# Kernel tuning notes

Hardware: AMD Instinct MI355X
Metric: run time of the kernel (lower is better)

Reference implementation:

```python
import jax, jax.numpy as jnp
import numpy as np

B, S, D, H = 2, 2048, 1024, 16
DK = D // H


def setup_inputs() -> dict:
    key = jax.random.key(0)
    ks = jax.random.split(key, 12)
    s = 0.02
    return {
        "q": jax.random.normal(ks[0], (B, S, D), jnp.float32),
        "k": jax.random.normal(ks[1], (B, S, D), jnp.float32),
        "v": jax.random.normal(ks[2], (B, S, D), jnp.float32),
        "mask": jax.random.randint(ks[3], (1, 1, S, S), 0, 2, jnp.int32),
        "Wq": jax.random.normal(ks[4], (D, D), jnp.float32) * s,
        "bq": jnp.zeros((D,), jnp.float32),
        "Wk": jax.random.normal(ks[5], (D, D), jnp.float32) * s,
        "bk": jnp.zeros((D,), jnp.float32),
        "Wv": jax.random.normal(ks[6], (D, D), jnp.float32) * s,
        "bv": jnp.zeros((D,), jnp.float32),
        "Wo": jax.random.normal(ks[7], (D, D), jnp.float32) * s,
        "bo": jnp.zeros((D,), jnp.float32),
    }


def reference(q, k, v, mask, Wq, bq, Wk, bk, Wv, bv, Wo, bo):
    # linear projections (torch Linear: x @ W.T + b)
    qp = q @ Wq.T + bq
    kp = k @ Wk.T + bk
    vp = v @ Wv.T + bv
    # [B, S, D] -> [B, H, S, DK]
    split = lambda x: x.reshape(B, S, H, DK).transpose(0, 2, 1, 3)
    qh, kh, vh = split(qp), split(kp), split(vp)
    scale = 1.0 / jnp.sqrt(jnp.float32(DK))
    attn = jnp.einsum('bhsd,bhtd->bhst', qh, kh) * scale  # [B,H,S,S]
    attn = jnp.where(mask == 0, jnp.float32(-1e9), attn)
    attn = jax.nn.softmax(attn, axis=-1)
    out = jnp.einsum('bhst,bhtd->bhsd', attn, vh)  # [B,H,S,DK]
    concat = out.transpose(0, 2, 1, 3).reshape(B, S, D)
    return concat @ Wo.T + bo
```

## Files before the change

### kernel.cpp

```cpp
#include <hip/hip_runtime.h>
#include <hip/hip_bf16.h>


using bf16x8 = __attribute__((ext_vector_type(8))) short;
using f32x4  = __attribute__((ext_vector_type(4))) float;

constexpr int Bc = 2, Sc = 2048, Dc = 1024, Hc = 16, DKc = 64;
constexpr int Mc = Bc * Sc;
#define LOG2E_OVER_SQRTDK 0.18033688011112042f

__device__ __forceinline__ void lds_load16(const void* g, void* l) {
  __builtin_amdgcn_global_load_lds(
      (const __attribute__((address_space(1))) unsigned int*)g,
      (__attribute__((address_space(3))) unsigned int*)l, 16, 0, 0);
}

__device__ __forceinline__ unsigned pack2bf(float a, float b) {
  union { __hip_bfloat16 h; unsigned short s; } ua, ub;
  ua.h = __float2bfloat16(a);
  ub.h = __float2bfloat16(b);
  return (unsigned)ua.s | ((unsigned)ub.s << 16);
}

__global__ void cast3_kernel(const float* __restrict__ a, const float* __restrict__ b,
                             const float* __restrict__ c, __hip_bfloat16* __restrict__ oa,
                             __hip_bfloat16* __restrict__ ob, __hip_bfloat16* __restrict__ oc2,
                             int n) {
  int gid = blockIdx.x * blockDim.x + threadIdx.x;
  int per = n >> 2;
  int which = gid / per, i = (gid - which * per) * 4;
  const float* s = which == 0 ? a : (which == 1 ? b : c);
  __hip_bfloat16* d = which == 0 ? oa : (which == 1 ? ob : oc2);
  float4 x = *(const float4*)&s[i];
  d[i + 0] = __float2bfloat16(x.x);
  d[i + 1] = __float2bfloat16(x.y);
  d[i + 2] = __float2bfloat16(x.z);
  d[i + 3] = __float2bfloat16(x.w);
}

__global__ void cast4_kernel(const float* __restrict__ a, const float* __restrict__ b,
                             const float* __restrict__ c, const float* __restrict__ dd,
                             __hip_bfloat16* __restrict__ oa, __hip_bfloat16* __restrict__ ob,
                             __hip_bfloat16* __restrict__ oc2, __hip_bfloat16* __restrict__ od,
                             int n) {
  int gid = blockIdx.x * blockDim.x + threadIdx.x;
  int per = n >> 2;
  int which = gid / per, i = (gid - which * per) * 4;
  const float* s = which == 0 ? a : (which == 1 ? b : (which == 2 ? c : dd));
  __hip_bfloat16* d = which == 0 ? oa : (which == 1 ? ob : (which == 2 ? oc2 : od));
  float4 x = *(const float4*)&s[i];
  d[i + 0] = __float2bfloat16(x.x);
  d[i + 1] = __float2bfloat16(x.y);
  d[i + 2] = __float2bfloat16(x.z);
  d[i + 3] = __float2bfloat16(x.w);
}

__global__ void mask_pack_kernel(const int* __restrict__ mask,
                                 unsigned long long* __restrict__ bits) {
  int i = blockIdx.x * blockDim.x + threadIdx.x;
  unsigned long long bal = __ballot(mask[i] != 0);
  if ((threadIdx.x & 63) == 0) bits[i >> 6] = bal;
}

__global__ __launch_bounds__(256) void gemm_bt(
    const __hip_bfloat16* __restrict__ X, const __hip_bfloat16* __restrict__ W,
    const float* __restrict__ bias, void* __restrict__ Y,
    int M, int N, int K, int mode, float scale) {
  __shared__ __align__(16) __hip_bfloat16 As[2][128 * 64];
  __shared__ __align__(16) __hip_bfloat16 Bs[2][64 * 64];
  const int tid = threadIdx.x;
  const int m0 = blockIdx.x * 128, n0 = blockIdx.y * 64;
  const int w = tid >> 6, lane = tid & 63, ln = lane & 15, quad = lane >> 4;
  const int wm = (w >> 1) * 64, wn = (w & 1) * 32;
  f32x4 acc[4][2] = {};

#define GEMM_STAGE(KB, BI)                                                    \
  {                                                                           \
    _Pragma("unroll") for (int i = 0; i < 4; ++i) {                           \
      int flat = (w * 4 + i) * 1024 + lane * 16;                              \
      int row = flat >> 7, cg = (flat >> 4) & 7;                              \
      lds_load16(&X[(size_t)(m0 + row) * K + (KB) + ((cg ^ (row & 7)) * 8)],  \
                 (char*)As[BI] + flat);                                       \
    }                                                                         \
    _Pragma("unroll") for (int i = 0; i < 2; ++i) {                           \
      int flat = (w * 2 + i) * 1024 + lane * 16;                              \
      int row = flat >> 7, cg = (flat >> 4) & 7;                              \
      lds_load16(&W[(size_t)(n0 + row) * K + (KB) + ((cg ^ (row & 7)) * 8)],  \
                 (char*)Bs[BI] + flat);                                       \
    }                                                                         \
  }

  GEMM_STAGE(0, 0);
  const int nkb = K / 64;
  for (int kb = 0; kb < nkb; ++kb) {
    const int bi = kb & 1;
    __syncthreads();
    if (kb + 1 < nkb) GEMM_STAGE((kb + 1) * 64, bi ^ 1);
    bf16x8 af[4][2], bf[2][2];
#pragma unroll
    for (int i = 0; i < 4; ++i) {
      int row = wm + i * 16 + ln;
#pragma unroll
      for (int kc = 0; kc < 2; ++kc)
        af[i][kc] = *(bf16x8*)((char*)As[bi] + row * 128 +
                               (((kc * 4 + quad) ^ (row & 7)) * 16));
    }
#pragma unroll
    for (int j = 0; j < 2; ++j) {
      int row = wn + j * 16 + ln;
#pragma unroll
      for (int kc = 0; kc < 2; ++kc)
        bf[j][kc] = *(bf16x8*)((char*)Bs[bi] + row * 128 +
                               (((kc * 4 + quad) ^ (row & 7)) * 16));
    }
#pragma unroll
    for (int i = 0; i < 4; ++i)
#pragma unroll
      for (int j = 0; j < 2; ++j)
#pragma unroll
        for (int kc = 0; kc < 2; ++kc)
          acc[i][j] = __builtin_amdgcn_mfma_f32_16x16x32_bf16(
              af[i][kc], bf[j][kc], acc[i][j], 0, 0, 0);
  }
#pragma unroll
  for (int i = 0; i < 4; ++i)
#pragma unroll
    for (int j = 0; j < 2; ++j) {
      int ng = n0 + wn + j * 16 + ln;
      int mbase = m0 + wm + i * 16 + quad * 4;
      float vv[4];
#pragma unroll
      for (int r = 0; r < 4; ++r) vv[r] = (acc[i][j][r] + bias[ng]) * scale;
      if (mode == 0) {
#pragma unroll
        for (int r = 0; r < 4; ++r) {
          int mg = mbase + r, b = mg >> 11, s = mg & 2047, h = ng >> 6, dk = ng & 63;
          ((__hip_bfloat16*)Y)[(((size_t)(b * Hc + h) * Sc + s) * DKc) + dk] =
              __float2bfloat16(vv[r]);
        }
      } else if (mode == 1) {
#pragma unroll
        for (int r = 0; r < 4; ++r)
          ((float*)Y)[(size_t)(mbase + r) * N + ng] = vv[r];
      } else {
        int b = mbase >> 11, s = mbase & 2047, h = ng >> 6, dk = ng & 63;
        uint2 pk = {pack2bf(vv[0], vv[1]), pack2bf(vv[2], vv[3])};
        *(uint2*)&((__hip_bfloat16*)Y)[(((size_t)(b * Hc + h) * DKc + dk) * Sc) + s] = pk;
      }
    }
}

__global__ __launch_bounds__(256) void flash_attn(
    const __hip_bfloat16* __restrict__ qh, const __hip_bfloat16* __restrict__ kh,
    const __hip_bfloat16* __restrict__ vt, const uint2* __restrict__ mbits,
    __hip_bfloat16* __restrict__ oc) {
  __shared__ __align__(16) __hip_bfloat16 Ks[2][64 * 64];
  __shared__ __align__(16) __hip_bfloat16 Vs[2][64 * 64];
  __shared__ __align__(16) __hip_bfloat16 Pt[4][32 * 72];
  const int tid = threadIdx.x;
  const int bh = blockIdx.y, b = bh >> 4, h = bh & 15;
  const int q0 = blockIdx.x * 128;
  const int w = tid >> 6, lane = tid & 63, ln = lane & 15, quad = lane >> 4;
  const size_t base = (size_t)bh * Sc * DKc;
  const __hip_bfloat16* khb = kh + base;
  const __hip_bfloat16* vtb = vt + base;
  char* ptw = (char*)&Pt[w][0];

  bf16x8 qf[2][2];
#pragma unroll
  for (int qt = 0; qt < 2; ++qt)
#pragma unroll
    for (int kc = 0; kc < 2; ++kc)
      qf[qt][kc] = *(const bf16x8*)&qh[base + (size_t)(q0 + w * 32 + qt * 16 + ln) * 64 +
                                       kc * 32 + quad * 8];

#define KV_STAGE(T0, BI)                                                      \
  {                                                                           \
    _Pragma("unroll") for (int i = 0; i < 2; ++i) {                           \
      int flat = (w * 2 + i) * 1024 + lane * 16;                              \
      int row = flat >> 7, cg = (flat >> 4) & 7;                              \
      int sw8 = (cg ^ (row & 7)) * 8;                                         \
      lds_load16(&khb[(size_t)((T0) + row) * 64 + sw8], (char*)Ks[BI] + flat);\
      lds_load16(&vtb[(size_t)row * Sc + (T0) + sw8], (char*)Vs[BI] + flat);  \
    }                                                                         \
  }

  KV_STAGE(0, 0);
  float lsum[2] = {0.f, 0.f};
  f32x4 Oacc[4][2] = {};

  for (int it = 0; it < Sc / 64; ++it) {
    const int bi = it & 1;
    __syncthreads();
    if (it + 1 < Sc / 64) KV_STAGE((it + 1) * 64, bi ^ 1);

    bf16x8 kf[4][2];
#pragma unroll
    for (int tt = 0; tt < 4; ++tt) {
      int row = tt * 16 + ln;
#pragma unroll
      for (int kc = 0; kc < 2; ++kc)
        kf[tt][kc] = *(bf16x8*)((char*)Ks[bi] + row * 128 +
                                (((kc * 4 + quad) ^ (row & 7)) * 16));
    }
    f32x4 sacc[2][4];
#pragma unroll
    for (int qt = 0; qt < 2; ++qt)
#pragma unroll
      for (int tt = 0; tt < 4; ++tt) {
        f32x4 a = {0.f, 0.f, 0.f, 0.f};
        a = __builtin_amdgcn_mfma_f32_16x16x32_bf16(kf[tt][0], qf[qt][0], a, 0, 0, 0);
        a = __builtin_amdgcn_mfma_f32_16x16x32_bf16(kf[tt][1], qf[qt][1], a, 0, 0, 0);
        sacc[qt][tt] = a;
      }
#pragma unroll
    for (int qt = 0; qt < 2; ++qt) {
      uint2 mw = mbits[(size_t)(q0 + w * 32 + qt * 16 + ln) * (Sc / 64) + it];
#pragma unroll
      for (int tt = 0; tt < 4; ++tt) {
        unsigned half = (tt & 2) ? mw.y : mw.x;
        unsigned pre = half >> ((tt & 1) * 16 + quad * 4);
        float p[4];
#pragma unroll
        for (int r = 0; r < 4; ++r) {
          float e = exp2f(sacc[qt][tt][r]);
          p[r] = (pre & (1u << r)) ? e : 0.f;
          lsum[qt] += p[r];
        }
        uint2 pk = {pack2bf(p[0], p[1]), pack2bf(p[2], p[3])};
        *(uint2*)(ptw + (qt * 16 + ln) * 144 + tt * 32 + quad * 8) = pk;
      }
    }
    bf16x8 vf[4][2], pb[2][2];
#pragma unroll
    for (int dt = 0; dt < 4; ++dt) {
      int row = dt * 16 + ln;
#pragma unroll
      for (int kc = 0; kc < 2; ++kc)
        vf[dt][kc] = *(bf16x8*)((char*)Vs[bi] + row * 128 +
                                (((kc * 4 + quad) ^ (row & 7)) * 16));
    }
#pragma unroll
    for (int qt = 0; qt < 2; ++qt)
#pragma unroll
      for (int kc = 0; kc < 2; ++kc)
        pb[qt][kc] = *(bf16x8*)(ptw + (qt * 16 + ln) * 144 + kc * 64 + quad * 16);
#pragma unroll
    for (int dt = 0; dt < 4; ++dt)
#pragma unroll
      for (int qt = 0; qt < 2; ++qt) {
        Oacc[dt][qt] = __builtin_amdgcn_mfma_f32_16x16x32_bf16(
            vf[dt][0], pb[qt][0], Oacc[dt][qt], 0, 0, 0);
        Oacc[dt][qt] = __builtin_amdgcn_mfma_f32_16x16x32_bf16(
            vf[dt][1], pb[qt][1], Oacc[dt][qt], 0, 0, 0);
      }
  }

  float linv[2];
#pragma unroll
  for (int qt = 0; qt < 2; ++qt) {
    float l = lsum[qt];
    l += __shfl_xor(l, 16);
    l += __shfl_xor(l, 32);
    linv[qt] = 1.f / fmaxf(l, 1e-30f);
  }
#pragma unroll
  for (int dt = 0; dt < 4; ++dt)
#pragma unroll
    for (int qt = 0; qt < 2; ++qt) {
      f32x4 o = Oacc[dt][qt];
      uint2 pk = {pack2bf(o[0] * linv[qt], o[1] * linv[qt]),
                  pack2bf(o[2] * linv[qt], o[3] * linv[qt])};
      *(uint2*)(ptw + (qt * 16 + ln) * 144 + dt * 32 + quad * 8) = pk;
    }
  __builtin_amdgcn_s_waitcnt(0);
#pragma unroll
  for (int chunk = 0; chunk < 4; ++chunk) {
    int row = chunk * 8 + (lane >> 3);
    bf16x8 val = *(bf16x8*)(ptw + row * 144 + (lane & 7) * 16);
    int s = q0 + w * 32 + row;
    *(bf16x8*)&oc[(size_t)(b * Sc + s) * Dc + h * 64 + (lane & 7) * 8] = val;
  }
}

extern "C" void kernel_launch(void* const* d_in, const int* in_sizes, int n_in,
                              void* d_out, int out_size, void* d_ws, size_t ws_size,
                              hipStream_t stream) {
  const float* q  = (const float*)d_in[0];
  const float* k  = (const float*)d_in[1];
  const float* v  = (const float*)d_in[2];
  const int* mask = (const int*)d_in[3];
  const float* Wq = (const float*)d_in[4];
  const float* bq = (const float*)d_in[5];
  const float* Wk = (const float*)d_in[6];
  const float* bk = (const float*)d_in[7];
  const float* Wv = (const float*)d_in[8];
  const float* bv = (const float*)d_in[9];
  const float* Wo = (const float*)d_in[10];
  const float* bo = (const float*)d_in[11];

  char* ws = (char*)d_ws;
  const size_t MB = 1024 * 1024;
  __hip_bfloat16* qb  = (__hip_bfloat16*)(ws + 0 * MB);
  unsigned long long* mbits = (unsigned long long*)(ws + 0 * MB);
  __hip_bfloat16* kb  = (__hip_bfloat16*)(ws + 8 * MB);
  __hip_bfloat16* vb  = (__hip_bfloat16*)(ws + 16 * MB);
  __hip_bfloat16* Wqb = (__hip_bfloat16*)(ws + 24 * MB);
  __hip_bfloat16* Wkb = (__hip_bfloat16*)(ws + 26 * MB);
  __hip_bfloat16* Wvb = (__hip_bfloat16*)(ws + 28 * MB);
  __hip_bfloat16* Wob = (__hip_bfloat16*)(ws + 30 * MB);
  __hip_bfloat16* qhd = (__hip_bfloat16*)(ws + 32 * MB);
  __hip_bfloat16* khd = (__hip_bfloat16*)(ws + 40 * MB);
  __hip_bfloat16* vtd = (__hip_bfloat16*)(ws + 48 * MB);
  __hip_bfloat16* oc  = (__hip_bfloat16*)(ws + 56 * MB);

  const int nQKV = Mc * Dc, nW = Dc * Dc;
  cast3_kernel<<<3 * (nQKV / 4) / 256, 256, 0, stream>>>(q, k, v, qb, kb, vb, nQKV);
  cast4_kernel<<<4 * (nW / 4) / 256, 256, 0, stream>>>(Wq, Wk, Wv, Wo, Wqb, Wkb,
                                                       Wvb, Wob, nW);

  dim3 gg(Mc / 128, Dc / 64);
  gemm_bt<<<gg, 256, 0, stream>>>(qb, Wqb, bq, qhd, Mc, Dc, Dc, 0, LOG2E_OVER_SQRTDK);
  mask_pack_kernel<<<(Sc * Sc) / 256, 256, 0, stream>>>(mask, mbits);
  gemm_bt<<<gg, 256, 0, stream>>>(kb, Wkb, bk, khd, Mc, Dc, Dc, 0, 1.0f);
  gemm_bt<<<gg, 256, 0, stream>>>(vb, Wvb, bv, vtd, Mc, Dc, Dc, 2, 1.0f);

  flash_attn<<<dim3(Sc / 128, Bc * Hc), 256, 0, stream>>>(
      qhd, khd, vtd, (const uint2*)mbits, oc);

  gemm_bt<<<gg, 256, 0, stream>>>(oc, Wob, bo, d_out, Mc, Dc, Dc, 1, 1.0f);
}
```

Measured before the change: 296.9 us.

## Fuse QKV projections into one GEMM and restructure flash attention pipeline

Replaces the three separate Q/K/V projection launches with one proj_qkv kernel that uses 128x128 tiles over a concatenated weight matrix and picks the input and bias per column block. Flash attention now uses one flat LDS buffer and an unrolled two-tile ping-pong loop that loads the mask 128 bits at a time. It also switches to a raw v_exp for exp2 and packs P to bf16 by truncation instead of rounding. The output GEMM gets precomputed swizzle offsets and launch-bounds occupancy hints. Risks: truncating P loses some precision, and the mask buffer moves to 8MB so it no longer shares space with qb. proj_qkv reads Wcat as one contiguous weight block, which depends on Wqb, Wkb and Wvb sitting next to each other in the workspace.

After: 251.3 us. 1.18x faster.

```diff
diff --git a/kernel.cpp b/kernel.cpp
--- a/kernel.cpp
+++ b/kernel.cpp
@@ -7,12 +7,26 @@
 
 constexpr int Bc = 2, Sc = 2048, Dc = 1024, Hc = 16, DKc = 64;
 constexpr int Mc = Bc * Sc;
-#define LOG2E_OVER_SQRTDK 0.18033688011112042f
+#define QSCALE 0.18033688011112042f
 
 __device__ __forceinline__ void lds_load16(const void* g, void* l) {
   __builtin_amdgcn_global_load_lds(
       (const __attribute__((address_space(1))) unsigned int*)g,
       (__attribute__((address_space(3))) unsigned int*)l, 16, 0, 0);
+}
+
+#if __has_builtin(__builtin_amdgcn_exp2f)
+__device__ __forceinline__ float exp2_fast(float x) { return __builtin_amdgcn_exp2f(x); }
+#else
+__device__ __forceinline__ float exp2_fast(float x) {
+  float r;
+  asm("v_exp_f32 %0, %1\n\ts_nop 0" : "=v"(r) : "v"(x));
+  return r;
+}
+#endif
+
+__device__ __forceinline__ unsigned pack_trunc(float a, float b) {
+  return __builtin_amdgcn_perm(__float_as_uint(b), __float_as_uint(a), 0x07060302u);
 }
 
 __device__ __forceinline__ unsigned pack2bf(float a, float b) {
@@ -62,65 +76,138 @@
   if ((threadIdx.x & 63) == 0) bits[i >> 6] = bal;
 }
 
-__global__ __launch_bounds__(256) void gemm_bt(
+__global__ __launch_bounds__(256, 3) void proj_qkv(
+    const __hip_bfloat16* __restrict__ qb, const __hip_bfloat16* __restrict__ kb,
+    const __hip_bfloat16* __restrict__ vb, const __hip_bfloat16* __restrict__ Wcat,
+    const float* __restrict__ bq, const float* __restrict__ bk,
+    const float* __restrict__ bv, __hip_bfloat16* __restrict__ qhd,
+    __hip_bfloat16* __restrict__ khd, __hip_bfloat16* __restrict__ vtd) {
+  __shared__ __align__(16) __hip_bfloat16 As[128 * 64];
+  __shared__ __align__(16) __hip_bfloat16 Bs[128 * 64];
+  const int tid = threadIdx.x;
+  const int m0 = blockIdx.x * 128, n0 = blockIdx.y * 128;
+  const int which = n0 >> 10, nl0 = n0 & 1023;
+  const __hip_bfloat16* X = which == 0 ? qb : (which == 1 ? kb : vb);
+  const float* bias = which == 0 ? bq : (which == 1 ? bk : bv);
+  const int w = tid >> 6, lane = tid & 63, ln = lane & 15, quad = lane >> 4;
+  const int swz = ((lane & 7) ^ (lane >> 3)) * 8;
+  const int rk0 = ln * 128 + ((quad ^ (ln & 7)) * 16);
+  const int rk1 = ln * 128 + (((quad + 4) ^ (ln & 7)) * 16);
+  const int aoff = (m0 + w * 32 + (lane >> 3)) * 1024 + swz;
+  const int boff = (n0 + w * 32 + (lane >> 3)) * 1024 + swz;
+  char* aF = (char*)As + (w >> 1) * 8192;
+  char* bF = (char*)Bs + (w & 1) * 8192;
+  char* aDst = (char*)As + w * 4096 + lane * 16;
+  char* bDst = (char*)Bs + w * 4096 + lane * 16;
+  f32x4 acc[4][4] = {};
+  int ko = 0;
+  for (int kb64 = 0; kb64 < 16; ++kb64, ko += 64) {
+#pragma unroll
+    for (int i = 0; i < 4; ++i) {
+      lds_load16(&X[aoff + i * 8192 + ko], aDst + i * 1024);
+      lds_load16(&Wcat[boff + i * 8192 + ko], bDst + i * 1024);
+    }
+    __syncthreads();
+    bf16x8 af[4][2], bf[4][2];
+#pragma unroll
+    for (int i = 0; i < 4; ++i) {
+      af[i][0] = *(bf16x8*)(aF + i * 2048 + rk0);
+      af[i][1] = *(bf16x8*)(aF + i * 2048 + rk1);
+      bf[i][0] = *(bf16x8*)(bF + i * 2048 + rk0);
+      bf[i][1] = *(bf16x8*)(bF + i * 2048 + rk1);
+    }
+#pragma unroll
+    for (int i = 0; i < 4; ++i)
+#pragma unroll
+      for (int j = 0; j < 4; ++j) {
+        acc[i][j] = __builtin_amdgcn_mfma_f32_16x16x32_bf16(af[i][0], bf[j][0],
+                                                            acc[i][j], 0, 0, 0);
+        acc[i][j] = __builtin_amdgcn_mfma_f32_16x16x32_bf16(af[i][1], bf[j][1],
+                                                            acc[i][j], 0, 0, 0);
+      }
+    __syncthreads();
+  }
+  const int wm = (w >> 1) * 64, wn = (w & 1) * 64;
+#pragma unroll
+  for (int i = 0; i < 4; ++i)
+#pragma unroll
+    for (int j = 0; j < 4; ++j) {
+      int ngl = nl0 + wn + j * 16 + ln;
+      int mbase = m0 + wm + i * 16 + quad * 4;
+      float bb = bias[ngl];
+      float vv[4];
+#pragma unroll
+      for (int r = 0; r < 4; ++r) vv[r] = acc[i][j][r] + bb;
+      int h = ngl >> 6, dk = ngl & 63;
+      int b = mbase >> 11, s = mbase & 2047;
+      if (which == 0) {
+#pragma unroll
+        for (int r = 0; r < 4; ++r)
+          qhd[(((size_t)(b * Hc + h) * Sc + s + r) * DKc) + dk] =
+              __float2bfloat16(vv[r] * QSCALE);
+      } else if (which == 1) {
+#pragma unroll
+        for (int r = 0; r < 4; ++r)
+          khd[(((size_t)(b * Hc + h) * Sc + s + r) * DKc) + dk] =
+              __float2bfloat16(vv[r]);
+      } else {
+        uint2 pk = {pack2bf(vv[0], vv[1]), pack2bf(vv[2], vv[3])};
+        *(uint2*)&vtd[(((size_t)(b * Hc + h) * DKc + dk) * Sc) + s] = pk;
+      }
+    }
+}
+
+__global__ __launch_bounds__(256, 2) void gemm_out(
     const __hip_bfloat16* __restrict__ X, const __hip_bfloat16* __restrict__ W,
-    const float* __restrict__ bias, void* __restrict__ Y,
-    int M, int N, int K, int mode, float scale) {
+    const float* __restrict__ bias, float* __restrict__ Y) {
   __shared__ __align__(16) __hip_bfloat16 As[2][128 * 64];
   __shared__ __align__(16) __hip_bfloat16 Bs[2][64 * 64];
   const int tid = threadIdx.x;
   const int m0 = blockIdx.x * 128, n0 = blockIdx.y * 64;
   const int w = tid >> 6, lane = tid & 63, ln = lane & 15, quad = lane >> 4;
   const int wm = (w >> 1) * 64, wn = (w & 1) * 32;
+  const int swz = ((lane & 7) ^ (lane >> 3)) * 8;
+  const int rk0 = ln * 128 + ((quad ^ (ln & 7)) * 16);
+  const int rk1 = ln * 128 + (((quad + 4) ^ (ln & 7)) * 16);
+  const int aoff = (m0 + w * 32 + (lane >> 3)) * 1024 + swz;
+  const int boff = (n0 + w * 16 + (lane >> 3)) * 1024 + swz;
   f32x4 acc[4][2] = {};
 
-#define GEMM_STAGE(KB, BI)                                                    \
+#define OSTAGE(KO, BI)                                                        \
   {                                                                           \
-    _Pragma("unroll") for (int i = 0; i < 4; ++i) {                           \
-      int flat = (w * 4 + i) * 1024 + lane * 16;                              \
-      int row = flat >> 7, cg = (flat >> 4) & 7;                              \
-      lds_load16(&X[(size_t)(m0 + row) * K + (KB) + ((cg ^ (row & 7)) * 8)],  \
-                 (char*)As[BI] + flat);                                       \
-    }                                                                         \
-    _Pragma("unroll") for (int i = 0; i < 2; ++i) {                           \
-      int flat = (w * 2 + i) * 1024 + lane * 16;                              \
-      int row = flat >> 7, cg = (flat >> 4) & 7;                              \
-      lds_load16(&W[(size_t)(n0 + row) * K + (KB) + ((cg ^ (row & 7)) * 8)],  \
-                 (char*)Bs[BI] + flat);                                       \
-    }                                                                         \
-  }
-
-  GEMM_STAGE(0, 0);
-  const int nkb = K / 64;
-  for (int kb = 0; kb < nkb; ++kb) {
-    const int bi = kb & 1;
+    _Pragma("unroll") for (int i = 0; i < 4; ++i)                             \
+        lds_load16(&X[aoff + i * 8192 + (KO)],                                \
+                   (char*)As[BI] + w * 4096 + lane * 16 + i * 1024);          \
+    _Pragma("unroll") for (int i = 0; i < 2; ++i)                             \
+        lds_load16(&W[boff + i * 8192 + (KO)],                                \
+                   (char*)Bs[BI] + w * 2048 + lane * 16 + i * 1024);          \
+  }
+
+  OSTAGE(0, 0);
+  for (int kb64 = 0; kb64 < 16; ++kb64) {
+    const int bi = kb64 & 1;
     __syncthreads();
-    if (kb + 1 < nkb) GEMM_STAGE((kb + 1) * 64, bi ^ 1);
+    if (kb64 + 1 < 16) OSTAGE((kb64 + 1) * 64, bi ^ 1);
     bf16x8 af[4][2], bf[2][2];
 #pragma unroll
     for (int i = 0; i < 4; ++i) {
-      int row = wm + i * 16 + ln;
-#pragma unroll
-      for (int kc = 0; kc < 2; ++kc)
-        af[i][kc] = *(bf16x8*)((char*)As[bi] + row * 128 +
-                               (((kc * 4 + quad) ^ (row & 7)) * 16));
+      af[i][0] = *(bf16x8*)((char*)As[bi] + wm * 128 + i * 2048 + rk0);
+      af[i][1] = *(bf16x8*)((char*)As[bi] + wm * 128 + i * 2048 + rk1);
     }
 #pragma unroll
     for (int j = 0; j < 2; ++j) {
-      int row = wn + j * 16 + ln;
-#pragma unroll
-      for (int kc = 0; kc < 2; ++kc)
-        bf[j][kc] = *(bf16x8*)((char*)Bs[bi] + row * 128 +
-                               (((kc * 4 + quad) ^ (row & 7)) * 16));
+      bf[j][0] = *(bf16x8*)((char*)Bs[bi] + wn * 128 + j * 2048 + rk0);
+      bf[j][1] = *(bf16x8*)((char*)Bs[bi] + wn * 128 + j * 2048 + rk1);
     }
 #pragma unroll
     for (int i = 0; i < 4; ++i)
 #pragma unroll
-      for (int j = 0; j < 2; ++j)
-#pragma unroll
-        for (int kc = 0; kc < 2; ++kc)
-          acc[i][j] = __builtin_amdgcn_mfma_f32_16x16x32_bf16(
-              af[i][kc], bf[j][kc], acc[i][j], 0, 0, 0);
+      for (int j = 0; j < 2; ++j) {
+        acc[i][j] = __builtin_amdgcn_mfma_f32_16x16x32_bf16(af[i][0], bf[j][0],
+                                                            acc[i][j], 0, 0, 0);
+        acc[i][j] = __builtin_amdgcn_mfma_f32_16x16x32_bf16(af[i][1], bf[j][1],
+                                                            acc[i][j], 0, 0, 0);
+      }
   }
 #pragma unroll
   for (int i = 0; i < 4; ++i)
@@ -128,35 +215,18 @@
     for (int j = 0; j < 2; ++j) {
       int ng = n0 + wn + j * 16 + ln;
       int mbase = m0 + wm + i * 16 + quad * 4;
-      float vv[4];
-#pragma unroll
-      for (int r = 0; r < 4; ++r) vv[r] = (acc[i][j][r] + bias[ng]) * scale;
-      if (mode == 0) {
-#pragma unroll
-        for (int r = 0; r < 4; ++r) {
-          int mg = mbase + r, b = mg >> 11, s = mg & 2047, h = ng >> 6, dk = ng & 63;
-          ((__hip_bfloat16*)Y)[(((size_t)(b * Hc + h) * Sc + s) * DKc) + dk] =
-              __float2bfloat16(vv[r]);
-        }
-      } else if (mode == 1) {
-#pragma unroll
-        for (int r = 0; r < 4; ++r)
-          ((float*)Y)[(size_t)(mbase + r) * N + ng] = vv[r];
-      } else {
-        int b = mbase >> 11, s = mbase & 2047, h = ng >> 6, dk = ng & 63;
-        uint2 pk = {pack2bf(vv[0], vv[1]), pack2bf(vv[2], vv[3])};
-        *(uint2*)&((__hip_bfloat16*)Y)[(((size_t)(b * Hc + h) * DKc + dk) * Sc) + s] = pk;
-      }
-    }
-}
-
-__global__ __launch_bounds__(256) void flash_attn(
+      float bb = bias[ng];
+#pragma unroll
+      for (int r = 0; r < 4; ++r)
+        Y[(size_t)(mbase + r) * Dc + ng] = acc[i][j][r] + bb;
+    }
+}
+
+__global__ __launch_bounds__(256, 2) void flash_attn(
     const __hip_bfloat16* __restrict__ qh, const __hip_bfloat16* __restrict__ kh,
-    const __hip_bfloat16* __restrict__ vt, const uint2* __restrict__ mbits,
+    const __hip_bfloat16* __restrict__ vt, const uint4* __restrict__ mb4,
     __hip_bfloat16* __restrict__ oc) {
-  __shared__ __align__(16) __hip_bfloat16 Ks[2][64 * 64];
-  __shared__ __align__(16) __hip_bfloat16 Vs[2][64 * 64];
-  __shared__ __align__(16) __hip_bfloat16 Pt[4][32 * 72];
+  __shared__ __align__(16) char L[51200];
   const int tid = threadIdx.x;
   const int bh = blockIdx.y, b = bh >> 4, h = bh & 15;
   const int q0 = blockIdx.x * 128;
@@ -164,96 +234,101 @@
   const size_t base = (size_t)bh * Sc * DKc;
   const __hip_bfloat16* khb = kh + base;
   const __hip_bfloat16* vtb = vt + base;
-  char* ptw = (char*)&Pt[w][0];
 
   bf16x8 qf[2][2];
 #pragma unroll
   for (int qt = 0; qt < 2; ++qt)
 #pragma unroll
     for (int kc = 0; kc < 2; ++kc)
-      qf[qt][kc] = *(const bf16x8*)&qh[base + (size_t)(q0 + w * 32 + qt * 16 + ln) * 64 +
-                                       kc * 32 + quad * 8];
-
-#define KV_STAGE(T0, BI)                                                      \
+      qf[qt][kc] = *(const bf16x8*)&qh[base +
+          (size_t)(q0 + w * 32 + qt * 16 + ln) * 64 + kc * 32 + quad * 8];
+
+  const int swz = ((lane & 7) ^ (lane >> 3)) * 8;
+  const int rk0 = ln * 128 + ((quad ^ (ln & 7)) * 16);
+  const int rk1 = ln * 128 + (((quad + 4) ^ (ln & 7)) * 16);
+  const int rPw = 32768 + w * 4608 + ln * 144 + quad * 8;
+  const int rPb = 32768 + w * 4608 + ln * 144 + quad * 16;
+  char* dmaL = L + w * 2048 + lane * 16;
+  int koff = (w * 16 + (lane >> 3)) * 64 + swz;
+  int voff0 = (w * 16 + (lane >> 3)) * Sc + swz;
+  int voff1 = voff0 + 8 * Sc;
+  int midx0 = (q0 + w * 32 + ln) * 16;
+  int midx1 = midx0 + 256;
+  const int sh0 = quad * 4, sh1 = quad * 4 + 16;
+
+#define KV_DMA(BI)                                                            \
   {                                                                           \
-    _Pragma("unroll") for (int i = 0; i < 2; ++i) {                           \
-      int flat = (w * 2 + i) * 1024 + lane * 16;                              \
-      int row = flat >> 7, cg = (flat >> 4) & 7;                              \
-      int sw8 = (cg ^ (row & 7)) * 8;                                         \
-      lds_load16(&khb[(size_t)((T0) + row) * 64 + sw8], (char*)Ks[BI] + flat);\
-      lds_load16(&vtb[(size_t)row * Sc + (T0) + sw8], (char*)Vs[BI] + flat);  \
-    }                                                                         \
-  }
-
-  KV_STAGE(0, 0);
+    lds_load16(khb + koff, dmaL + (BI)*8192);                                 \
+    lds_load16(khb + koff + 512, dmaL + (BI)*8192 + 1024);                    \
+    lds_load16(vtb + voff0, dmaL + 16384 + (BI)*8192);                        \
+    lds_load16(vtb + voff1, dmaL + 16384 + (BI)*8192 + 1024);                 \
+  }
+
   float lsum[2] = {0.f, 0.f};
   f32x4 Oacc[4][2] = {};
-
-  for (int it = 0; it < Sc / 64; ++it) {
-    const int bi = it & 1;
+  KV_DMA(0);
+
+#define FTILE(BUF, LO0, HI0, LO1, HI1)                                        \
+  {                                                                           \
+    bf16x8 kf[4][2];                                                          \
+    _Pragma("unroll") for (int tt = 0; tt < 4; ++tt) {                        \
+      kf[tt][0] = *(bf16x8*)(L + (BUF)*8192 + tt * 2048 + rk0);               \
+      kf[tt][1] = *(bf16x8*)(L + (BUF)*8192 + tt * 2048 + rk1);               \
+    }                                                                         \
+    _Pragma("unroll") for (int qt = 0; qt < 2; ++qt) {                        \
+      f32x4 s[4];                                                             \
+      _Pragma("unroll") for (int tt = 0; tt < 4; ++tt) {                      \
+        f32x4 z = {0.f, 0.f, 0.f, 0.f};                                       \
+        z = __builtin_amdgcn_mfma_f32_16x16x32_bf16(kf[tt][0], qf[qt][0], z,  \
+                                                    0, 0, 0);                 \
+        s[tt] = __builtin_amdgcn_mfma_f32_16x16x32_bf16(kf[tt][1], qf[qt][1], \
+                                                        z, 0, 0, 0);          \
+      }                                                                       \
+      unsigned lo = qt ? (LO1) : (LO0), hi = qt ? (HI1) : (HI0);              \
+      _Pragma("unroll") for (int tt = 0; tt < 4; ++tt) {                      \
+        unsigned word = (tt & 2) ? hi : lo;                                   \
+        unsigned pre = word >> ((tt & 1) ? sh1 : sh0);                        \
+        float p[4];                                                           \
+        _Pragma("unroll") for (int r = 0; r < 4; ++r) {                       \
+          float e = exp2_fast(s[tt][r]);                                      \
+          p[r] = (pre & (1u << r)) ? e : 0.f;                                 \
+          lsum[qt] += p[r];                                                   \
+        }                                                                     \
+        uint2 pk = {pack_trunc(p[0], p[1]), pack_trunc(p[2], p[3])};          \
+        *(uint2*)(L + rPw + qt * 2304 + tt * 32) = pk;                        \
+      }                                                                       \
+    }                                                                         \
+    bf16x8 vf[4][2], pb[2][2];                                                \
+    _Pragma("unroll") for (int dt = 0; dt < 4; ++dt) {                        \
+      vf[dt][0] = *(bf16x8*)(L + 16384 + (BUF)*8192 + dt * 2048 + rk0);       \
+      vf[dt][1] = *(bf16x8*)(L + 16384 + (BUF)*8192 + dt * 2048 + rk1);       \
+    }                                                                         \
+    _Pragma("unroll") for (int qt = 0; qt < 2; ++qt) {                        \
+      pb[qt][0] = *(bf16x8*)(L + rPb + qt * 2304);                            \
+      pb[qt][1] = *(bf16x8*)(L + rPb + qt * 2304 + 64);                       \
+    }                                                                         \
+    _Pragma("unroll") for (int dt = 0; dt < 4; ++dt)                          \
+        _Pragma("unroll") for (int qt = 0; qt < 2; ++qt) {                    \
+      Oacc[dt][qt] = __builtin_amdgcn_mfma_f32_16x16x32_bf16(                 \
+          vf[dt][0], pb[qt][0], Oacc[dt][qt], 0, 0, 0);                       \
+      Oacc[dt][qt] = __builtin_amdgcn_mfma_f32_16x16x32_bf16(                 \
+          vf[dt][1], pb[qt][1], Oacc[dt][qt], 0, 0, 0);                       \
+    }                                                                         \
+  }
+
+  for (int it2 = 0; it2 < 16; ++it2) {
     __syncthreads();
-    if (it + 1 < Sc / 64) KV_STAGE((it + 1) * 64, bi ^ 1);
-
-    bf16x8 kf[4][2];
-#pragma unroll
-    for (int tt = 0; tt < 4; ++tt) {
-      int row = tt * 16 + ln;
-#pragma unroll
-      for (int kc = 0; kc < 2; ++kc)
-        kf[tt][kc] = *(bf16x8*)((char*)Ks[bi] + row * 128 +
-                                (((kc * 4 + quad) ^ (row & 7)) * 16));
-    }
-    f32x4 sacc[2][4];
-#pragma unroll
-    for (int qt = 0; qt < 2; ++qt)
-#pragma unroll
-      for (int tt = 0; tt < 4; ++tt) {
-        f32x4 a = {0.f, 0.f, 0.f, 0.f};
-        a = __builtin_amdgcn_mfma_f32_16x16x32_bf16(kf[tt][0], qf[qt][0], a, 0, 0, 0);
-        a = __builtin_amdgcn_mfma_f32_16x16x32_bf16(kf[tt][1], qf[qt][1], a, 0, 0, 0);
-        sacc[qt][tt] = a;
-      }
-#pragma unroll
-    for (int qt = 0; qt < 2; ++qt) {
-      uint2 mw = mbits[(size_t)(q0 + w * 32 + qt * 16 + ln) * (Sc / 64) + it];
-#pragma unroll
-      for (int tt = 0; tt < 4; ++tt) {
-        unsigned half = (tt & 2) ? mw.y : mw.x;
-        unsigned pre = half >> ((tt & 1) * 16 + quad * 4);
-        float p[4];
-#pragma unroll
-        for (int r = 0; r < 4; ++r) {
-          float e = exp2f(sacc[qt][tt][r]);
-          p[r] = (pre & (1u << r)) ? e : 0.f;
-          lsum[qt] += p[r];
-        }
-        uint2 pk = {pack2bf(p[0], p[1]), pack2bf(p[2], p[3])};
-        *(uint2*)(ptw + (qt * 16 + ln) * 144 + tt * 32 + quad * 8) = pk;
-      }
-    }
-    bf16x8 vf[4][2], pb[2][2];
-#pragma unroll
-    for (int dt = 0; dt < 4; ++dt) {
-      int row = dt * 16 + ln;
-#pragma unroll
-      for (int kc = 0; kc < 2; ++kc)
-        vf[dt][kc] = *(bf16x8*)((char*)Vs[bi] + row * 128 +
-                                (((kc * 4 + quad) ^ (row & 7)) * 16));
-    }
-#pragma unroll
-    for (int qt = 0; qt < 2; ++qt)
-#pragma unroll
-      for (int kc = 0; kc < 2; ++kc)
-        pb[qt][kc] = *(bf16x8*)(ptw + (qt * 16 + ln) * 144 + kc * 64 + quad * 16);
-#pragma unroll
-    for (int dt = 0; dt < 4; ++dt)
-#pragma unroll
-      for (int qt = 0; qt < 2; ++qt) {
-        Oacc[dt][qt] = __builtin_amdgcn_mfma_f32_16x16x32_bf16(
-            vf[dt][0], pb[qt][0], Oacc[dt][qt], 0, 0, 0);
-        Oacc[dt][qt] = __builtin_amdgcn_mfma_f32_16x16x32_bf16(
-            vf[dt][1], pb[qt][1], Oacc[dt][qt], 0, 0, 0);
-      }
+    uint4 mq0 = mb4[midx0], mq1 = mb4[midx1];
+    ++midx0; ++midx1;
+    koff += 4096; voff0 += 64; voff1 += 64;
+    KV_DMA(1);
+    FTILE(0, mq0.x, mq0.y, mq1.x, mq1.y);
+    __syncthreads();
+    if (it2 < 15) {
+      koff += 4096; voff0 += 64; voff1 += 64;
+      KV_DMA(0);
+    }
+    FTILE(1, mq0.z, mq0.w, mq1.z, mq1.w);
   }
 
   float linv[2];
@@ -271,13 +346,13 @@
       f32x4 o = Oacc[dt][qt];
       uint2 pk = {pack2bf(o[0] * linv[qt], o[1] * linv[qt]),
                   pack2bf(o[2] * linv[qt], o[3] * linv[qt])};
-      *(uint2*)(ptw + (qt * 16 + ln) * 144 + dt * 32 + quad * 8) = pk;
+      *(uint2*)(L + rPw + qt * 2304 + dt * 32) = pk;
     }
   __builtin_amdgcn_s_waitcnt(0);
 #pragma unroll
   for (int chunk = 0; chunk < 4; ++chunk) {
     int row = chunk * 8 + (lane >> 3);
-    bf16x8 val = *(bf16x8*)(ptw + row * 144 + (lane & 7) * 16);
+    bf16x8 val = *(bf16x8*)(L + 32768 + w * 4608 + row * 144 + (lane & 7) * 16);
     int s = q0 + w * 32 + row;
     *(bf16x8*)&oc[(size_t)(b * Sc + s) * Dc + h * 64 + (lane & 7) * 8] = val;
   }
@@ -302,8 +377,8 @@
   char* ws = (char*)d_ws;
   const size_t MB = 1024 * 1024;
   __hip_bfloat16* qb  = (__hip_bfloat16*)(ws + 0 * MB);
-  unsigned long long* mbits = (unsigned long long*)(ws + 0 * MB);
   __hip_bfloat16* kb  = (__hip_bfloat16*)(ws + 8 * MB);
+  unsigned long long* mbits = (unsigned long long*)(ws + 8 * MB);
   __hip_bfloat16* vb  = (__hip_bfloat16*)(ws + 16 * MB);
   __hip_bfloat16* Wqb = (__hip_bfloat16*)(ws + 24 * MB);
   __hip_bfloat16* Wkb = (__hip_bfloat16*)(ws + 26 * MB);
@@ -319,14 +394,13 @@
   cast4_kernel<<<4 * (nW / 4) / 256, 256, 0, stream>>>(Wq, Wk, Wv, Wo, Wqb, Wkb,
                                                        Wvb, Wob, nW);
 
-  dim3 gg(Mc / 128, Dc / 64);
-  gemm_bt<<<gg, 256, 0, stream>>>(qb, Wqb, bq, qhd, Mc, Dc, Dc, 0, LOG2E_OVER_SQRTDK);
+  proj_qkv<<<dim3(Mc / 128, 3 * Dc / 128), 256, 0, stream>>>(
+      qb, kb, vb, Wqb, bq, bk, bv, qhd, khd, vtd);
+
   mask_pack_kernel<<<(Sc * Sc) / 256, 256, 0, stream>>>(mask, mbits);
-  gemm_bt<<<gg, 256, 0, stream>>>(kb, Wkb, bk, khd, Mc, Dc, Dc, 0, 1.0f);
-  gemm_bt<<<gg, 256, 0, stream>>>(vb, Wvb, bv, vtd, Mc, Dc, Dc, 2, 1.0f);
 
   flash_attn<<<dim3(Sc / 128, Bc * Hc), 256, 0, stream>>>(
-      qhd, khd, vtd, (const uint2*)mbits, oc);
-
-  gemm_bt<<<gg, 256, 0, stream>>>(oc, Wob, bo, d_out, Mc, Dc, Dc, 1, 1.0f);
-}
+      qhd, khd, vtd, (const uint4*)mbits, oc);
+
+  gemm_out<<<dim3(Mc / 128, Dc / 64), 256, 0, stream>>>(oc, Wob, bo, (float*)d_out);
+}
```
